# Performance work log

Hardware: AMD Instinct MI355X
Metric: run time of the kernel (lower is better)

The kernel has to match this reference:

```python
import jax, jax.numpy as jnp
import numpy as np

B, T, J = 256, 150, 25  # batch, time_step, num_joints (NTU-style skeleton)
K_LIST = (2, 3, 4)      # k values from the source loop -> 3 stats each -> topo_feat_dim = 9


def setup_inputs() -> dict:
    key = jax.random.key(0)
    x = jax.random.normal(key, (B, T, J, 3), dtype=jnp.float32)
    return {"x": x}


def _pairwise_dist(pos):
    # pos: [B,T,J,3] -> dist: [B,T,J,J], safe sqrt so grad at zero diagonal is 0
    diff = pos[:, :, :, None, :] - pos[:, :, None, :, :]          # [B,T,J,J,3]
    s = jnp.sum(diff * diff, axis=-1)                              # [B,T,J,J]
    return jnp.where(s > 0, jnp.sqrt(jnp.where(s > 0, s, 1.0)), 0.0)


def reference(x) -> jnp.ndarray:
    # Faithful, fully vectorized version of the topo-feature block of
    # FiveStreamMaha_GCN_Model.forward (per-frame cdist + kNN + stats),
    # batched over all frames instead of Python loops over t and k.
    pos = x[..., :3]                     # [B,T,J,3]
    dist = _pairwise_dist(pos)           # [B,T,J,J]

    feats = []
    for k in K_LIST:
        actual_k = min(k, J - 1)
        # smallest (actual_k+1) distances; drop self (distance 0 at index 0)
        neg_vals, _ = jax.lax.top_k(-dist, actual_k + 1)   # [B,T,J,k+1], descending in -d
        knn_d = -neg_vals[..., 1:actual_k + 1]             # [B,T,J,k], ascending distances
        avg_dist = jnp.mean(knn_d, axis=-1)                # [B,T,J]
        std_dist = jnp.std(knn_d, axis=-1, ddof=1)         # torch.std default: unbiased
        min_dist = jnp.min(knn_d, axis=-1)                 # [B,T,J]
        k_feat = jnp.stack([avg_dist, std_dist, min_dist], axis=-1)  # [B,T,J,3]
        feats.append(jnp.mean(k_feat, axis=1))             # mean over time -> [B,J,3]

    return jnp.concatenate(feats, axis=-1)                 # [B,J,9]
```

## Files before the change

### kernel.cpp

```cpp
#include <hip/hip_runtime.h>
#include <cfloat>

#define NB 256
#define NT 150
#define NJ 25
#define CHUNK 6
#define CPB (NT / CHUNK)
#define WAVES 4
#define BLOCKSZ 256
#define NW (NB * CPB)

#define FSQRT(x) __builtin_amdgcn_sqrtf(x)

#define INS4(s0, s1, s2, s3, v)                                   \
    {                                                             \
        float m_;                                                 \
        m_ = fminf(s0, v); v = fmaxf(s0, v); s0 = m_;             \
        m_ = fminf(s1, v); v = fmaxf(s1, v); s1 = m_;             \
        m_ = fminf(s2, v); v = fmaxf(s2, v); s2 = m_;             \
        s3 = fminf(s3, v);                                        \
    }

__global__ __launch_bounds__(BLOCKSZ, 4) void knn_partial_kernel(
        const float* __restrict__ x, float* __restrict__ ws) {
    __shared__ float4 spos[WAVES][CHUNK][NJ];

    const int tid  = threadIdx.x;
    const int wave = tid >> 6;
    const int lane = tid & 63;
    const int half = lane >> 5;
    const int jj   = lane & 31;
    const bool act = (jj < NJ);

    const int gw = blockIdx.x * WAVES + wave;
    const int b  = gw / CPB;
    const int c  = gw - b * CPB;
    const int t0 = c * CHUNK;

    const float* src = x + (size_t)(b * NT + t0) * NJ * 3;
    for (int p = lane; p < CHUNK * NJ; p += 64) {
        const int f = p / NJ;
        const int j = p - f * NJ;
        const float* s = src + p * 3;
        spos[wave][f][j] = make_float4(s[0], s[1], s[2], 0.0f);
    }
    __syncthreads();

    float acc[9];
#pragma unroll
    for (int f = 0; f < 9; ++f) acc[f] = 0.0f;

#pragma unroll 1
    for (int p = 0; p < CHUNK / 2; ++p) {
        const int fr = 2 * p + half;
        const float4 own = spos[wave][fr][act ? jj : 0];

        float a0 = FLT_MAX, a1 = FLT_MAX, a2 = FLT_MAX, a3 = FLT_MAX;
        float e0 = FLT_MAX, e1 = FLT_MAX, e2 = FLT_MAX, e3 = FLT_MAX;
#pragma unroll
        for (int i = 0; i < 13; ++i) {
            const float4 q = spos[wave][fr][i];
            const float dx = q.x - own.x, dy = q.y - own.y, dz = q.z - own.z;
            float d2 = dx * dx + dy * dy + dz * dz;
            d2 = (i == jj) ? FLT_MAX : d2;
            INS4(a0, a1, a2, a3, d2);
        }
#pragma unroll
        for (int i = 13; i < NJ; ++i) {
            const float4 q = spos[wave][fr][i];
            const float dx = q.x - own.x, dy = q.y - own.y, dz = q.z - own.z;
            float d2 = dx * dx + dy * dy + dz * dz;
            d2 = (i == jj) ? FLT_MAX : d2;
            INS4(e0, e1, e2, e3, d2);
        }
        const float l0 = fminf(a0, e3), l1 = fminf(a1, e2);
        const float l2 = fminf(a2, e1), l3 = fminf(a3, e0);
        const float m0 = fminf(l0, l2), m2 = fmaxf(l0, l2);
        const float m1 = fminf(l1, l3), m3 = fmaxf(l1, l3);
        const float r0 = fminf(m0, m1), r1 = fmaxf(m0, m1);
        const float r2 = fminf(m2, m3), r3 = fmaxf(m2, m3);

        const float d1 = FSQRT(r0), d2r = FSQRT(r1);
        const float d3 = FSQRT(r2), d4 = FSQRT(r3);

        const float rs2 = r0 + r1, rs3 = rs2 + r2, rs4 = rs3 + r3;
        const float s2 = d1 + d2r, a2f = 0.5f * s2;
        acc[0] += a2f;
        acc[1] += FSQRT(fmaxf(rs2 - 2.0f * a2f * a2f, 0.0f));
        acc[2] += d1;
        const float s3 = s2 + d3, a3f = s3 * (1.0f / 3.0f);
        acc[3] += a3f;
        acc[4] += FSQRT(fmaxf((rs3 - 3.0f * a3f * a3f) * 0.5f, 0.0f));
        acc[5] += d1;
        const float s4 = s3 + d4, a4f = 0.25f * s4;
        acc[6] += a4f;
        acc[7] += FSQRT(fmaxf((rs4 - 4.0f * a4f * a4f) * (1.0f / 3.0f), 0.0f));
        acc[8] += d1;
    }

#pragma unroll
    for (int f = 0; f < 9; ++f) acc[f] += __shfl_xor(acc[f], 32, 64);

    if (act && half == 0) {
        float* op = ws + (size_t)gw * 225;
#pragma unroll
        for (int f = 0; f < 9; ++f) op[f * NJ + jj] = acc[f];
    }
}

__global__ __launch_bounds__(BLOCKSZ) void reduce_kernel(
        const float* __restrict__ ws, float* __restrict__ out) {
    const int i = blockIdx.x * blockDim.x + threadIdx.x;
    if (i >= NB * NJ * 9) return;
    const int b = i / 225;
    const int r = i - b * 225;
    float s = 0.0f;
#pragma unroll
    for (int c = 0; c < CPB; ++c) s += ws[(size_t)(b * CPB + c) * 225 + r];
    const int f = r / NJ;
    const int j = r - f * NJ;
    out[b * 225 + j * 9 + f] = s * (1.0f / (float)NT);
}

extern "C" void kernel_launch(void* const* d_in, const int* in_sizes, int n_in,
                              void* d_out, int out_size, void* d_ws, size_t ws_size,
                              hipStream_t stream) {
    const float* x = (const float*)d_in[0];
    float* out = (float*)d_out;
    float* ws = (float*)d_ws;

    knn_partial_kernel<<<NW / WAVES, BLOCKSZ, 0, stream>>>(x, ws);
    reduce_kernel<<<(NB * NJ * 9 + BLOCKSZ - 1) / BLOCKSZ, BLOCKSZ, 0, stream>>>(ws, out);
}
```

Before: 76.26 us.

## Remap kNN work to half-sequence blocks with two joints per lane

Each block now handles half of a batch's time steps and loops over 16-frame slots with shared-memory staging. Each lane handles two joints over all 25 candidates, where before two lanes split one joint's candidates and merged their lists. The redundant min feature is computed once, and partials are reduced in-block to a 7-value workspace, which shrinks the second kernel's work. The trade-offs are fewer blocks (512), padded wasted slots in the last iteration, and extra block syncs per iteration.

```diff
diff --git a/kernel.cpp b/kernel.cpp
--- a/kernel.cpp
+++ b/kernel.cpp
@@ -4,11 +4,10 @@
 #define NB 256
 #define NT 150
 #define NJ 25
-#define CHUNK 6
-#define CPB (NT / CHUNK)
-#define WAVES 4
+#define HALF_T 75
+#define SLOTS 16
+#define ITERS 5
 #define BLOCKSZ 256
-#define NW (NB * CPB)
 
 #define FSQRT(x) __builtin_amdgcn_sqrtf(x)
 
@@ -21,105 +20,133 @@
         s3 = fminf(s3, v);                                        \
     }
 
-__global__ __launch_bounds__(BLOCKSZ, 4) void knn_partial_kernel(
+__device__ __forceinline__ void features(float r0, float r1, float r2, float r3,
+                                         float* f) {
+    const float d1 = FSQRT(r0), d2 = FSQRT(r1), d3 = FSQRT(r2), d4 = FSQRT(r3);
+    const float rs2 = r0 + r1, rs3 = rs2 + r2, rs4 = rs3 + r3;
+    const float s2 = d1 + d2, a2f = 0.5f * s2;
+    const float s3 = s2 + d3, a3f = s3 * (1.0f / 3.0f);
+    const float s4 = s3 + d4, a4f = 0.25f * s4;
+    f[0] = a2f;
+    f[1] = FSQRT(fmaxf(rs2 - 2.0f * a2f * a2f, 0.0f));
+    f[2] = a3f;
+    f[3] = FSQRT(fmaxf((rs3 - 3.0f * a3f * a3f) * 0.5f, 0.0f));
+    f[4] = a4f;
+    f[5] = FSQRT(fmaxf((rs4 - 4.0f * a4f * a4f) * (1.0f / 3.0f), 0.0f));
+    f[6] = d1;
+}
+
+__global__ __launch_bounds__(BLOCKSZ, 4) void knn_feat(
         const float* __restrict__ x, float* __restrict__ ws) {
-    __shared__ float4 spos[WAVES][CHUNK][NJ];
+    __shared__ float4 spos[SLOTS][NJ];
+    __shared__ float  red[4][16][14];
 
     const int tid  = threadIdx.x;
     const int wave = tid >> 6;
     const int lane = tid & 63;
-    const int half = lane >> 5;
-    const int jj   = lane & 31;
-    const bool act = (jj < NJ);
+    const int q    = (lane >> 4) & 3;
+    const int k    = lane & 15;
+    const int slot = wave * 4 + q;
+    const int jj0  = min(2 * k, NJ - 1);
+    const int jj1  = min(2 * k + 1, NJ - 1);
 
-    const int gw = blockIdx.x * WAVES + wave;
-    const int b  = gw / CPB;
-    const int c  = gw - b * CPB;
-    const int t0 = c * CHUNK;
+    const int blk = blockIdx.x;
+    const int b   = blk >> 1;
+    const int h   = blk & 1;
+    const float* xb = x + (size_t)(b * NT + h * HALF_T) * NJ * 3;
 
-    const float* src = x + (size_t)(b * NT + t0) * NJ * 3;
-    for (int p = lane; p < CHUNK * NJ; p += 64) {
-        const int f = p / NJ;
-        const int j = p - f * NJ;
-        const float* s = src + p * 3;
-        spos[wave][f][j] = make_float4(s[0], s[1], s[2], 0.0f);
-    }
-    __syncthreads();
-
-    float acc[9];
+    float acc0[7], acc1[7];
 #pragma unroll
-    for (int f = 0; f < 9; ++f) acc[f] = 0.0f;
+    for (int f = 0; f < 7; ++f) { acc0[f] = 0.0f; acc1[f] = 0.0f; }
 
 #pragma unroll 1
-    for (int p = 0; p < CHUNK / 2; ++p) {
-        const int fr = 2 * p + half;
-        const float4 own = spos[wave][fr][act ? jj : 0];
+    for (int it = 0; it < ITERS; ++it) {
+#pragma unroll
+        for (int turn = 0; turn < 2; ++turn) {
+            const int t = tid + turn * BLOCKSZ;
+            if (t < SLOTS * NJ) {
+                const int fl = t / NJ;
+                const int j  = t - fl * NJ;
+                const int gf = min(it * SLOTS + fl, HALF_T - 1);
+                const float* s = xb + (size_t)(gf * NJ + j) * 3;
+                spos[fl][j] = make_float4(s[0], s[1], s[2], 0.0f);
+            }
+        }
+        __syncthreads();
+
+        const float4 own0 = spos[slot][jj0];
+        const float4 own1 = spos[slot][jj1];
 
         float a0 = FLT_MAX, a1 = FLT_MAX, a2 = FLT_MAX, a3 = FLT_MAX;
         float e0 = FLT_MAX, e1 = FLT_MAX, e2 = FLT_MAX, e3 = FLT_MAX;
 #pragma unroll
-        for (int i = 0; i < 13; ++i) {
-            const float4 q = spos[wave][fr][i];
-            const float dx = q.x - own.x, dy = q.y - own.y, dz = q.z - own.z;
-            float d2 = dx * dx + dy * dy + dz * dz;
-            d2 = (i == jj) ? FLT_MAX : d2;
-            INS4(a0, a1, a2, a3, d2);
+        for (int i = 0; i < NJ; ++i) {
+            const float4 c = spos[slot][i];
+            float dx = c.x - own0.x, dy = c.y - own0.y, dz = c.z - own0.z;
+            float d20 = dx * dx + dy * dy + dz * dz;
+            dx = c.x - own1.x; dy = c.y - own1.y; dz = c.z - own1.z;
+            float d21 = dx * dx + dy * dy + dz * dz;
+            d20 = (i == jj0) ? FLT_MAX : d20;
+            d21 = (i == jj1) ? FLT_MAX : d21;
+            INS4(a0, a1, a2, a3, d20);
+            INS4(e0, e1, e2, e3, d21);
         }
+
+        float f0[7], f1[7];
+        features(a0, a1, a2, a3, f0);
+        features(e0, e1, e2, e3, f1);
+
+        const float vm = (it * SLOTS + slot < HALF_T) ? 1.0f : 0.0f;
 #pragma unroll
-        for (int i = 13; i < NJ; ++i) {
-            const float4 q = spos[wave][fr][i];
-            const float dx = q.x - own.x, dy = q.y - own.y, dz = q.z - own.z;
-            float d2 = dx * dx + dy * dy + dz * dz;
-            d2 = (i == jj) ? FLT_MAX : d2;
-            INS4(e0, e1, e2, e3, d2);
+        for (int f = 0; f < 7; ++f) {
+            acc0[f] = fmaf(vm, f0[f], acc0[f]);
+            acc1[f] = fmaf(vm, f1[f], acc1[f]);
         }
-        const float l0 = fminf(a0, e3), l1 = fminf(a1, e2);
-        const float l2 = fminf(a2, e1), l3 = fminf(a3, e0);
-        const float m0 = fminf(l0, l2), m2 = fmaxf(l0, l2);
-        const float m1 = fminf(l1, l3), m3 = fmaxf(l1, l3);
-        const float r0 = fminf(m0, m1), r1 = fmaxf(m0, m1);
-        const float r2 = fminf(m2, m3), r3 = fmaxf(m2, m3);
-
-        const float d1 = FSQRT(r0), d2r = FSQRT(r1);
-        const float d3 = FSQRT(r2), d4 = FSQRT(r3);
-
-        const float rs2 = r0 + r1, rs3 = rs2 + r2, rs4 = rs3 + r3;
-        const float s2 = d1 + d2r, a2f = 0.5f * s2;
-        acc[0] += a2f;
-        acc[1] += FSQRT(fmaxf(rs2 - 2.0f * a2f * a2f, 0.0f));
-        acc[2] += d1;
-        const float s3 = s2 + d3, a3f = s3 * (1.0f / 3.0f);
-        acc[3] += a3f;
-        acc[4] += FSQRT(fmaxf((rs3 - 3.0f * a3f * a3f) * 0.5f, 0.0f));
-        acc[5] += d1;
-        const float s4 = s3 + d4, a4f = 0.25f * s4;
-        acc[6] += a4f;
-        acc[7] += FSQRT(fmaxf((rs4 - 4.0f * a4f * a4f) * (1.0f / 3.0f), 0.0f));
-        acc[8] += d1;
+        __syncthreads();
     }
 
 #pragma unroll
-    for (int f = 0; f < 9; ++f) acc[f] += __shfl_xor(acc[f], 32, 64);
+    for (int f = 0; f < 7; ++f) {
+        acc0[f] += __shfl_xor(acc0[f], 16, 64);
+        acc0[f] += __shfl_xor(acc0[f], 32, 64);
+        acc1[f] += __shfl_xor(acc1[f], 16, 64);
+        acc1[f] += __shfl_xor(acc1[f], 32, 64);
+    }
+    if (lane < 16) {
+#pragma unroll
+        for (int f = 0; f < 7; ++f) {
+            red[wave][k][f]     = acc0[f];
+            red[wave][k][7 + f] = acc1[f];
+        }
+    }
+    __syncthreads();
 
-    if (act && half == 0) {
-        float* op = ws + (size_t)gw * 225;
-#pragma unroll
-        for (int f = 0; f < 9; ++f) op[f * NJ + jj] = acc[f];
+    if (tid < 16 * 14) {
+        const int k2   = tid / 14;
+        const int rest = tid - k2 * 14;
+        const int which = rest / 7;
+        const int f    = rest - which * 7;
+        const int j    = 2 * k2 + which;
+        if (j < NJ) {
+            const float s = red[0][k2][rest] + red[1][k2][rest] +
+                            red[2][k2][rest] + red[3][k2][rest];
+            ws[(size_t)((b * 2 + h) * NJ + j) * 7 + f] = s * (1.0f / (float)NT);
+        }
     }
 }
 
-__global__ __launch_bounds__(BLOCKSZ) void reduce_kernel(
+__global__ __launch_bounds__(BLOCKSZ) void final_kernel(
         const float* __restrict__ ws, float* __restrict__ out) {
-    const int i = blockIdx.x * blockDim.x + threadIdx.x;
-    if (i >= NB * NJ * 9) return;
-    const int b = i / 225;
-    const int r = i - b * 225;
-    float s = 0.0f;
-#pragma unroll
-    for (int c = 0; c < CPB; ++c) s += ws[(size_t)(b * CPB + c) * 225 + r];
-    const int f = r / NJ;
-    const int j = r - f * NJ;
-    out[b * 225 + j * 9 + f] = s * (1.0f / (float)NT);
+    const int o = blockIdx.x * blockDim.x + threadIdx.x;
+    if (o >= NB * NJ * 9) return;
+    const int f9 = o % 9;
+    const int bj = o / 9;
+    const int j  = bj % NJ;
+    const int b  = bj / NJ;
+    const int f7 = (f9 % 3 == 2) ? 6 : (f9 / 3) * 2 + (f9 % 3);
+    const size_t i0 = (size_t)((b * 2 + 0) * NJ + j) * 7 + f7;
+    const size_t i1 = (size_t)((b * 2 + 1) * NJ + j) * 7 + f7;
+    out[o] = ws[i0] + ws[i1];
 }
 
 extern "C" void kernel_launch(void* const* d_in, const int* in_sizes, int n_in,
@@ -129,6 +156,6 @@
     float* out = (float*)d_out;
     float* ws = (float*)d_ws;
 
-    knn_partial_kernel<<<NW / WAVES, BLOCKSZ, 0, stream>>>(x, ws);
-    reduce_kernel<<<(NB * NJ * 9 + BLOCKSZ - 1) / BLOCKSZ, BLOCKSZ, 0, stream>>>(ws, out);
+    knn_feat<<<NB * 2, BLOCKSZ, 0, stream>>>(x, ws);
+    final_kernel<<<(NB * NJ * 9 + BLOCKSZ - 1) / BLOCKSZ, BLOCKSZ, 0, stream>>>(ws, out);
 }
```

New measurement: 74.27 us. 1.03x faster.
